# Optimization experiments

Measured on AMD Instinct MI355X. Metric: run time of the kernel, lower is better.

The kernel has to match this reference:

```python
import jax
import jax.numpy as jnp
import numpy as np

L, H_DIM = 8192, 128
ATTN_WINDOW, STRIDE = 3, 2


def setup_inputs() -> dict:
    key = jax.random.key(0)
    k1, k2, k3, k4, k5 = jax.random.split(key, 5)
    input_sequence = jax.random.normal(k1, (L, H_DIM), dtype=jnp.float32)
    # zoh-discretized diagonal decays exp(Lambda*Delta) lie in (0,1)
    Lambda_bar = jax.random.uniform(k2, (H_DIM, H_DIM), dtype=jnp.float32,
                                    minval=0.5, maxval=0.999)
    C_tilde = jax.random.normal(k3, (H_DIM, H_DIM), dtype=jnp.float32) / jnp.sqrt(
        jnp.float32(H_DIM))
    w_q = jax.random.normal(k4, (ATTN_WINDOW, ATTN_WINDOW), dtype=jnp.float32) * 0.1
    D = jax.random.normal(k5, (ATTN_WINDOW,), dtype=jnp.float32)
    return {
        "input_sequence": input_sequence,
        "Lambda_bar": Lambda_bar,
        "C_tilde": C_tilde,
        "w_q": w_q,
        "D": D,
        "attn_window": ATTN_WINDOW,
        "stride": STRIDE,
    }


def reference(input_sequence, Lambda_bar, C_tilde, w_q, D, attn_window, stride):
    # input_sequence: (L, H); Lambda_bar, C_tilde: (H, H); w_q: (W, W); D: (W,)
    Lseq, H = input_sequence.shape
    num_windows = (Lseq - attn_window) // stride + 1
    idx = jnp.arange(num_windows)[:, None] * stride + jnp.arange(attn_window)
    windows = input_sequence[idx]  # (T, W, H)

    # local self-attention per window: x.T @ w_q @ x  -> (T, H, H), axes (t, a, d)
    lsa = jnp.einsum("twa,wv,tvd->tad", windows, w_q, windows)

    # diagonal linear SSM scan over windows, vectorized over both H axes:
    # carry[a, d] = Lambda_bar[a, d] * carry[a, d] + lsa[t, a, d]
    def step(carry, inp):
        carry = Lambda_bar * carry + inp
        return carry, carry

    init = jnp.zeros((H, H), dtype=input_sequence.dtype)
    _, zs = jax.lax.scan(step, init, lsa)  # (T, a, d)

    # original stacks per-d scans on axis=1 giving (T, d, a), then C_tilde @ u
    # contracts d: out[t, h, a] = sum_d C_tilde[h, d] * zs[t, a, d]
    zs_out = jnp.einsum("hd,tad->tha", C_tilde, zs)  # (T, H, H)

    # os = vmap(u.T @ D): (T, H)
    os = jnp.einsum("twh,w->th", windows, D)
    return zs_out, os
```

## Files before the change

kernel.cpp:

```cpp
#include <hip/hip_runtime.h>

#define L_   8192
#define H_   128
#define T_   4095
#define CH_  16
#define NC_  256

typedef __bf16 bf16x8 __attribute__((ext_vector_type(8)));
typedef unsigned short ushort8 __attribute__((ext_vector_type(8)));
typedef float f32x4 __attribute__((ext_vector_type(4)));

__device__ __forceinline__ unsigned short f2bf(float f) {
    unsigned int u = __builtin_bit_cast(unsigned int, f);
    u += 0x7fffu + ((u >> 16) & 1u);
    return (unsigned short)(u >> 16);
}

__global__ __launch_bounds__(256) void pass1_kernel(const float* __restrict__ X,
                                                    const float* __restrict__ Lam,
                                                    const float* __restrict__ wq,
                                                    float* __restrict__ ebuf) {
    __shared__ float y_s[3][128];
    __shared__ float xa_s[3][32];

    const int tid = threadIdx.x;
    const int c   = blockIdx.x;
    const int a0  = blockIdx.y * 32;
    const int a_l = tid & 31;
    const int dg  = tid >> 5;

    float z[16], lam[16];
    {
        const float* lp = Lam + (size_t)(a0 + a_l) * H_ + dg * 16;
        #pragma unroll
        for (int j = 0; j < 16; ++j) { lam[j] = lp[j]; z[j] = 0.f; }
    }
    const float w00 = wq[0], w01 = wq[1], w02 = wq[2];
    const float w10 = wq[3], w11 = wq[4], w12 = wq[5];
    const float w20 = wq[6], w21 = wq[7], w22 = wq[8];

    const int t0 = c * CH_;
    const int t1 = min(t0 + CH_, T_);

    for (int t = t0; t < t1; ++t) {
        __syncthreads();
        const float* xr = X + (size_t)(2 * t) * H_;
        if (tid < 128) {
            float xd0 = xr[tid], xd1 = xr[H_ + tid], xd2 = xr[2 * H_ + tid];
            y_s[0][tid] = w00 * xd0 + w01 * xd1 + w02 * xd2;
            y_s[1][tid] = w10 * xd0 + w11 * xd1 + w12 * xd2;
            y_s[2][tid] = w20 * xd0 + w21 * xd1 + w22 * xd2;
        } else if (tid < 224) {
            int li = tid - 128;
            xa_s[li >> 5][li & 31] = xr[(li >> 5) * H_ + a0 + (li & 31)];
        }
        __syncthreads();
        const float xa0 = xa_s[0][a_l], xa1 = xa_s[1][a_l], xa2 = xa_s[2][a_l];
        #pragma unroll
        for (int j = 0; j < 16; ++j) {
            const int d = dg * 16 + j;
            float u = xa0 * y_s[0][d] + xa1 * y_s[1][d] + xa2 * y_s[2][d];
            z[j] = fmaf(lam[j], z[j], u);
        }
    }
    float* ep = ebuf + (size_t)c * (H_ * H_) + (size_t)(a0 + a_l) * H_ + dg * 16;
    #pragma unroll
    for (int j = 0; j < 16; ++j) ep[j] = z[j];
}

__global__ __launch_bounds__(256) void pass2_kernel(const float* __restrict__ Lam,
                                                    float* __restrict__ ebuf) {
    const int entry = blockIdx.x * 256 + threadIdx.x;
    const float lam = Lam[entry];
    float p = lam * lam; p = p * p; p = p * p; p = p * p;
    float z = 0.f;
    for (int cb = 0; cb < NC_; cb += 8) {
        float tmp[8];
        #pragma unroll
        for (int i = 0; i < 8; ++i)
            tmp[i] = ebuf[(size_t)(cb + i) * (H_ * H_) + entry];
        #pragma unroll
        for (int i = 0; i < 8; ++i) {
            ebuf[(size_t)(cb + i) * (H_ * H_) + entry] = z;
            z = fmaf(p, z, tmp[i]);
        }
    }
}

__global__ __launch_bounds__(256) void pass3_kernel(const float* __restrict__ X,
                                                    const float* __restrict__ Lam,
                                                    const float* __restrict__ Cm,
                                                    const float* __restrict__ wq,
                                                    const float* __restrict__ Dv,
                                                    const float* __restrict__ carry,
                                                    float* __restrict__ out,
                                                    float* __restrict__ os) {
    __shared__ unsigned short z_s[32][136];
    __shared__ float y_s[3][128];
    __shared__ float xa_s[3][32];

    const int tid  = threadIdx.x;
    const int c    = blockIdx.x;
    const int a0   = blockIdx.y * 32;
    const int lane = tid & 63;
    const int wave = tid >> 6;
    const int m    = lane & 15;
    const int q    = lane >> 4;

    ushort8 cfrag[2][4];
    #pragma unroll
    for (int ni = 0; ni < 2; ++ni) {
        const int h = (wave * 2 + ni) * 16 + m;
        #pragma unroll
        for (int kt = 0; kt < 4; ++kt) {
            const float* src = Cm + h * H_ + kt * 32 + q * 8;
            ushort8 v;
            #pragma unroll
            for (int j = 0; j < 8; ++j) v[j] = f2bf(src[j]);
            cfrag[ni][kt] = v;
        }
    }

    const int a_l = tid & 31;
    const int dg  = tid >> 5;
    float z[16], lam[16];
    {
        const float* lp = Lam   + (size_t)(a0 + a_l) * H_ + dg * 16;
        const float* cp = carry + (size_t)c * (H_ * H_) + (size_t)(a0 + a_l) * H_ + dg * 16;
        #pragma unroll
        for (int j = 0; j < 16; ++j) { lam[j] = lp[j]; z[j] = cp[j]; }
    }
    const float w00 = wq[0], w01 = wq[1], w02 = wq[2];
    const float w10 = wq[3], w11 = wq[4], w12 = wq[5];
    const float w20 = wq[6], w21 = wq[7], w22 = wq[8];
    const float d0 = Dv[0], d1 = Dv[1], d2 = Dv[2];
    const bool do_os = (blockIdx.y == 0);

    const int t0 = c * CH_;
    const int t1 = min(t0 + CH_, T_);

    for (int t = t0; t < t1; ++t) {
        __syncthreads();
        const float* xr = X + (size_t)(2 * t) * H_;
        if (tid < 128) {
            float xd0 = xr[tid], xd1 = xr[H_ + tid], xd2 = xr[2 * H_ + tid];
            y_s[0][tid] = w00 * xd0 + w01 * xd1 + w02 * xd2;
            y_s[1][tid] = w10 * xd0 + w11 * xd1 + w12 * xd2;
            y_s[2][tid] = w20 * xd0 + w21 * xd1 + w22 * xd2;
            if (do_os) os[t * H_ + tid] = d0 * xd0 + d1 * xd1 + d2 * xd2;
        } else if (tid < 224) {
            int li = tid - 128;
            xa_s[li >> 5][li & 31] = xr[(li >> 5) * H_ + a0 + (li & 31)];
        }
        __syncthreads();

        {
            const float xa0 = xa_s[0][a_l], xa1 = xa_s[1][a_l], xa2 = xa_s[2][a_l];
            #pragma unroll
            for (int j = 0; j < 16; ++j) {
                const int d = dg * 16 + j;
                float u = xa0 * y_s[0][d] + xa1 * y_s[1][d] + xa2 * y_s[2][d];
                z[j] = fmaf(lam[j], z[j], u);
            }
            ushort8 zb0, zb1;
            #pragma unroll
            for (int j = 0; j < 8; ++j) { zb0[j] = f2bf(z[j]); zb1[j] = f2bf(z[j + 8]); }
            *(ushort8*)&z_s[a_l][dg * 16]     = zb0;
            *(ushort8*)&z_s[a_l][dg * 16 + 8] = zb1;
        }
        __syncthreads();

        f32x4 acc[2][2] = {};
        #pragma unroll
        for (int kt = 0; kt < 4; ++kt) {
            bf16x8 za = __builtin_bit_cast(bf16x8, *(const ushort8*)&z_s[m][kt * 32 + q * 8]);
            bf16x8 zb = __builtin_bit_cast(bf16x8, *(const ushort8*)&z_s[16 + m][kt * 32 + q * 8]);
            #pragma unroll
            for (int ni = 0; ni < 2; ++ni) {
                bf16x8 cf = __builtin_bit_cast(bf16x8, cfrag[ni][kt]);
                acc[0][ni] = __builtin_amdgcn_mfma_f32_16x16x32_bf16(za, cf, acc[0][ni], 0, 0, 0);
                acc[1][ni] = __builtin_amdgcn_mfma_f32_16x16x32_bf16(zb, cf, acc[1][ni], 0, 0, 0);
            }
        }
        float* ob = out + (size_t)t * (H_ * H_) + a0;
        #pragma unroll
        for (int mi = 0; mi < 2; ++mi) {
            #pragma unroll
            for (int ni = 0; ni < 2; ++ni) {
                const int h = (wave * 2 + ni) * 16 + m;
                *(f32x4*)&ob[(size_t)h * H_ + mi * 16 + q * 4] = acc[mi][ni];
            }
        }
    }
}

extern "C" void kernel_launch(void* const* d_in, const int* in_sizes, int n_in,
                              void* d_out, int out_size, void* d_ws, size_t ws_size,
                              hipStream_t stream) {
    const float* X   = (const float*)d_in[0];
    const float* Lam = (const float*)d_in[1];
    const float* Cm  = (const float*)d_in[2];
    const float* wq  = (const float*)d_in[3];
    const float* Dv  = (const float*)d_in[4];
    float* out = (float*)d_out;
    float* os  = out + (size_t)T_ * H_ * H_;
    float* ebuf = (float*)d_ws;

    pass1_kernel<<<dim3(NC_, 4), 256, 0, stream>>>(X, Lam, wq, ebuf);
    pass2_kernel<<<64, 256, 0, stream>>>(Lam, ebuf);
    pass3_kernel<<<dim3(NC_, 4), 256, 0, stream>>>(X, Lam, Cm, wq, Dv, ebuf, out, os);
}
```

Before: 346.6 us.

## Restructure scan passes into sync-free single-wave blocks with precomputed bf16 C fragments

Pass1 and pass3 drop shared memory and barriers. Each thread now loads X rows directly with vector loads and recomputes the w_q projection itself. Pass3 becomes 64-thread blocks over 16-row tiles that keep the bf16 z fragment in registers and feed it straight into MFMA, and a new pass0 pre-packs C into bf16 MFMA fragment layout in workspace. Pass1 skips the last chunk and pass2 turns into an inclusive scan read with a shifted index, which removes unused work. The trade-off is redundant X loads and y computation per thread, plus C fragments reloaded from global memory every timestep.

```diff
diff --git a/kernel.cpp b/kernel.cpp
--- a/kernel.cpp
+++ b/kernel.cpp
@@ -5,6 +5,8 @@
 #define T_   4095
 #define CH_  16
 #define NC_  256
+#define HH_  (H_ * H_)
+#define CBF_OFF ((size_t)(NC_ - 1) * HH_)
 
 typedef __bf16 bf16x8 __attribute__((ext_vector_type(8)));
 typedef unsigned short ushort8 __attribute__((ext_vector_type(8)));
@@ -16,180 +18,184 @@
     return (unsigned short)(u >> 16);
 }
 
+__global__ __launch_bounds__(256) void pass0_kernel(const float* __restrict__ Cm,
+                                                    unsigned short* __restrict__ Cbf) {
+    const int gid  = blockIdx.x * 256 + threadIdx.x;
+    const int frag = gid >> 6, lane = gid & 63;
+    const int nt = frag >> 2, kt = frag & 3;
+    const int n  = nt * 16 + (lane & 15);
+    const int k0 = kt * 32 + (lane >> 4) * 8;
+    const float* src = Cm + (size_t)n * H_ + k0;
+    ushort8 v;
+    #pragma unroll
+    for (int j = 0; j < 8; ++j) v[j] = f2bf(src[j]);
+    *(ushort8*)(Cbf + (size_t)gid * 8) = v;
+}
+
 __global__ __launch_bounds__(256) void pass1_kernel(const float* __restrict__ X,
                                                     const float* __restrict__ Lam,
                                                     const float* __restrict__ wq,
                                                     float* __restrict__ ebuf) {
-    __shared__ float y_s[3][128];
-    __shared__ float xa_s[3][32];
-
     const int tid = threadIdx.x;
     const int c   = blockIdx.x;
-    const int a0  = blockIdx.y * 32;
-    const int a_l = tid & 31;
-    const int dg  = tid >> 5;
-
-    float z[16], lam[16];
+    const int a0  = blockIdx.y * 16;
+    const int a   = a0 + (tid & 15);
+    const int d0  = (tid >> 4) * 8;
+
+    float z[8], lam[8];
     {
-        const float* lp = Lam + (size_t)(a0 + a_l) * H_ + dg * 16;
-        #pragma unroll
-        for (int j = 0; j < 16; ++j) { lam[j] = lp[j]; z[j] = 0.f; }
+        const float* lp = Lam + (size_t)a * H_ + d0;
+        #pragma unroll
+        for (int j = 0; j < 8; ++j) { lam[j] = lp[j]; z[j] = 0.f; }
     }
     const float w00 = wq[0], w01 = wq[1], w02 = wq[2];
     const float w10 = wq[3], w11 = wq[4], w12 = wq[5];
     const float w20 = wq[6], w21 = wq[7], w22 = wq[8];
 
     const int t0 = c * CH_;
-    const int t1 = min(t0 + CH_, T_);
-
-    for (int t = t0; t < t1; ++t) {
-        __syncthreads();
+    for (int t = t0; t < t0 + CH_; ++t) {
         const float* xr = X + (size_t)(2 * t) * H_;
-        if (tid < 128) {
-            float xd0 = xr[tid], xd1 = xr[H_ + tid], xd2 = xr[2 * H_ + tid];
-            y_s[0][tid] = w00 * xd0 + w01 * xd1 + w02 * xd2;
-            y_s[1][tid] = w10 * xd0 + w11 * xd1 + w12 * xd2;
-            y_s[2][tid] = w20 * xd0 + w21 * xd1 + w22 * xd2;
-        } else if (tid < 224) {
-            int li = tid - 128;
-            xa_s[li >> 5][li & 31] = xr[(li >> 5) * H_ + a0 + (li & 31)];
-        }
-        __syncthreads();
-        const float xa0 = xa_s[0][a_l], xa1 = xa_s[1][a_l], xa2 = xa_s[2][a_l];
-        #pragma unroll
-        for (int j = 0; j < 16; ++j) {
-            const int d = dg * 16 + j;
-            float u = xa0 * y_s[0][d] + xa1 * y_s[1][d] + xa2 * y_s[2][d];
-            z[j] = fmaf(lam[j], z[j], u);
-        }
-    }
-    float* ep = ebuf + (size_t)c * (H_ * H_) + (size_t)(a0 + a_l) * H_ + dg * 16;
-    #pragma unroll
-    for (int j = 0; j < 16; ++j) ep[j] = z[j];
+        f32x4 x0a = *(const f32x4*)(xr + d0),           x0b = *(const f32x4*)(xr + d0 + 4);
+        f32x4 x1a = *(const f32x4*)(xr + H_ + d0),      x1b = *(const f32x4*)(xr + H_ + d0 + 4);
+        f32x4 x2a = *(const f32x4*)(xr + 2 * H_ + d0),  x2b = *(const f32x4*)(xr + 2 * H_ + d0 + 4);
+        const float xa0 = xr[a], xa1 = xr[H_ + a], xa2 = xr[2 * H_ + a];
+        #pragma unroll
+        for (int j = 0; j < 4; ++j) {
+            {
+                const float y0 = w00 * x0a[j] + w01 * x1a[j] + w02 * x2a[j];
+                const float y1 = w10 * x0a[j] + w11 * x1a[j] + w12 * x2a[j];
+                const float y2 = w20 * x0a[j] + w21 * x1a[j] + w22 * x2a[j];
+                z[j] = fmaf(lam[j], z[j], xa0 * y0 + xa1 * y1 + xa2 * y2);
+            }
+            {
+                const float y0 = w00 * x0b[j] + w01 * x1b[j] + w02 * x2b[j];
+                const float y1 = w10 * x0b[j] + w11 * x1b[j] + w12 * x2b[j];
+                const float y2 = w20 * x0b[j] + w21 * x1b[j] + w22 * x2b[j];
+                z[j + 4] = fmaf(lam[j + 4], z[j + 4], xa0 * y0 + xa1 * y1 + xa2 * y2);
+            }
+        }
+    }
+    float* ep = ebuf + (size_t)c * HH_ + (size_t)a * H_ + d0;
+    f32x4 zlo = {z[0], z[1], z[2], z[3]};
+    f32x4 zhi = {z[4], z[5], z[6], z[7]};
+    *(f32x4*)ep       = zlo;
+    *(f32x4*)(ep + 4) = zhi;
 }
 
 __global__ __launch_bounds__(256) void pass2_kernel(const float* __restrict__ Lam,
                                                     float* __restrict__ ebuf) {
-    const int entry = blockIdx.x * 256 + threadIdx.x;
-    const float lam = Lam[entry];
-    float p = lam * lam; p = p * p; p = p * p; p = p * p;
+    const int e = blockIdx.x * 256 + threadIdx.x;
+    const float lam = Lam[e];
+    float p2 = lam * lam, p4 = p2 * p2, p8 = p4 * p4;
+    const float l16 = p8 * p8;
     float z = 0.f;
-    for (int cb = 0; cb < NC_; cb += 8) {
+    for (int cb = 0; cb < 248; cb += 8) {
         float tmp[8];
         #pragma unroll
-        for (int i = 0; i < 8; ++i)
-            tmp[i] = ebuf[(size_t)(cb + i) * (H_ * H_) + entry];
+        for (int i = 0; i < 8; ++i) tmp[i] = ebuf[(size_t)(cb + i) * HH_ + e];
         #pragma unroll
         for (int i = 0; i < 8; ++i) {
-            ebuf[(size_t)(cb + i) * (H_ * H_) + entry] = z;
-            z = fmaf(p, z, tmp[i]);
-        }
-    }
-}
-
-__global__ __launch_bounds__(256) void pass3_kernel(const float* __restrict__ X,
-                                                    const float* __restrict__ Lam,
-                                                    const float* __restrict__ Cm,
-                                                    const float* __restrict__ wq,
-                                                    const float* __restrict__ Dv,
-                                                    const float* __restrict__ carry,
-                                                    float* __restrict__ out,
-                                                    float* __restrict__ os) {
-    __shared__ unsigned short z_s[32][136];
-    __shared__ float y_s[3][128];
-    __shared__ float xa_s[3][32];
-
-    const int tid  = threadIdx.x;
+            z = fmaf(l16, z, tmp[i]);
+            ebuf[(size_t)(cb + i) * HH_ + e] = z;
+        }
+    }
+    {
+        float tmp[7];
+        #pragma unroll
+        for (int i = 0; i < 7; ++i) tmp[i] = ebuf[(size_t)(248 + i) * HH_ + e];
+        #pragma unroll
+        for (int i = 0; i < 7; ++i) {
+            z = fmaf(l16, z, tmp[i]);
+            ebuf[(size_t)(248 + i) * HH_ + e] = z;
+        }
+    }
+}
+
+__global__ __launch_bounds__(64, 2) void pass3_kernel(const float* __restrict__ X,
+                                                      const float* __restrict__ Lam,
+                                                      const float* __restrict__ wq,
+                                                      const float* __restrict__ Dv,
+                                                      const float* __restrict__ ws,
+                                                      float* __restrict__ out,
+                                                      float* __restrict__ os) {
+    const int lane = threadIdx.x;
     const int c    = blockIdx.x;
-    const int a0   = blockIdx.y * 32;
-    const int lane = tid & 63;
-    const int wave = tid >> 6;
-    const int m    = lane & 15;
-    const int q    = lane >> 4;
-
-    ushort8 cfrag[2][4];
+    const int a0   = blockIdx.y * 16;
+    const int m    = lane & 15, q = lane >> 4;
+    const int a    = a0 + m;
+    const unsigned short* Cbf = (const unsigned short*)(ws + CBF_OFF);
+
+    float z[4][8], lam[4][8];
     #pragma unroll
-    for (int ni = 0; ni < 2; ++ni) {
-        const int h = (wave * 2 + ni) * 16 + m;
-        #pragma unroll
-        for (int kt = 0; kt < 4; ++kt) {
-            const float* src = Cm + h * H_ + kt * 32 + q * 8;
-            ushort8 v;
-            #pragma unroll
-            for (int j = 0; j < 8; ++j) v[j] = f2bf(src[j]);
-            cfrag[ni][kt] = v;
-        }
-    }
-
-    const int a_l = tid & 31;
-    const int dg  = tid >> 5;
-    float z[16], lam[16];
-    {
-        const float* lp = Lam   + (size_t)(a0 + a_l) * H_ + dg * 16;
-        const float* cp = carry + (size_t)c * (H_ * H_) + (size_t)(a0 + a_l) * H_ + dg * 16;
-        #pragma unroll
-        for (int j = 0; j < 16; ++j) { lam[j] = lp[j]; z[j] = cp[j]; }
+    for (int cc = 0; cc < 4; ++cc) {
+        const int k0 = cc * 32 + q * 8;
+        const float* lp = Lam + (size_t)a * H_ + k0;
+        #pragma unroll
+        for (int j = 0; j < 8; ++j) lam[cc][j] = lp[j];
+        if (c == 0) {
+            #pragma unroll
+            for (int j = 0; j < 8; ++j) z[cc][j] = 0.f;
+        } else {
+            const float* cp = ws + (size_t)(c - 1) * HH_ + (size_t)a * H_ + k0;
+            #pragma unroll
+            for (int j = 0; j < 8; ++j) z[cc][j] = cp[j];
+        }
     }
     const float w00 = wq[0], w01 = wq[1], w02 = wq[2];
     const float w10 = wq[3], w11 = wq[4], w12 = wq[5];
     const float w20 = wq[6], w21 = wq[7], w22 = wq[8];
-    const float d0 = Dv[0], d1 = Dv[1], d2 = Dv[2];
+    const float dv0 = Dv[0], dv1 = Dv[1], dv2 = Dv[2];
     const bool do_os = (blockIdx.y == 0);
 
-    const int t0 = c * CH_;
-    const int t1 = min(t0 + CH_, T_);
-
+    const int t0 = c * CH_, t1 = min(t0 + CH_, T_);
     for (int t = t0; t < t1; ++t) {
-        __syncthreads();
         const float* xr = X + (size_t)(2 * t) * H_;
-        if (tid < 128) {
-            float xd0 = xr[tid], xd1 = xr[H_ + tid], xd2 = xr[2 * H_ + tid];
-            y_s[0][tid] = w00 * xd0 + w01 * xd1 + w02 * xd2;
-            y_s[1][tid] = w10 * xd0 + w11 * xd1 + w12 * xd2;
-            y_s[2][tid] = w20 * xd0 + w21 * xd1 + w22 * xd2;
-            if (do_os) os[t * H_ + tid] = d0 * xd0 + d1 * xd1 + d2 * xd2;
-        } else if (tid < 224) {
-            int li = tid - 128;
-            xa_s[li >> 5][li & 31] = xr[(li >> 5) * H_ + a0 + (li & 31)];
-        }
-        __syncthreads();
-
-        {
-            const float xa0 = xa_s[0][a_l], xa1 = xa_s[1][a_l], xa2 = xa_s[2][a_l];
-            #pragma unroll
-            for (int j = 0; j < 16; ++j) {
-                const int d = dg * 16 + j;
-                float u = xa0 * y_s[0][d] + xa1 * y_s[1][d] + xa2 * y_s[2][d];
-                z[j] = fmaf(lam[j], z[j], u);
-            }
-            ushort8 zb0, zb1;
-            #pragma unroll
-            for (int j = 0; j < 8; ++j) { zb0[j] = f2bf(z[j]); zb1[j] = f2bf(z[j + 8]); }
-            *(ushort8*)&z_s[a_l][dg * 16]     = zb0;
-            *(ushort8*)&z_s[a_l][dg * 16 + 8] = zb1;
-        }
-        __syncthreads();
-
-        f32x4 acc[2][2] = {};
-        #pragma unroll
-        for (int kt = 0; kt < 4; ++kt) {
-            bf16x8 za = __builtin_bit_cast(bf16x8, *(const ushort8*)&z_s[m][kt * 32 + q * 8]);
-            bf16x8 zb = __builtin_bit_cast(bf16x8, *(const ushort8*)&z_s[16 + m][kt * 32 + q * 8]);
-            #pragma unroll
-            for (int ni = 0; ni < 2; ++ni) {
-                bf16x8 cf = __builtin_bit_cast(bf16x8, cfrag[ni][kt]);
-                acc[0][ni] = __builtin_amdgcn_mfma_f32_16x16x32_bf16(za, cf, acc[0][ni], 0, 0, 0);
-                acc[1][ni] = __builtin_amdgcn_mfma_f32_16x16x32_bf16(zb, cf, acc[1][ni], 0, 0, 0);
-            }
-        }
-        float* ob = out + (size_t)t * (H_ * H_) + a0;
-        #pragma unroll
-        for (int mi = 0; mi < 2; ++mi) {
-            #pragma unroll
-            for (int ni = 0; ni < 2; ++ni) {
-                const int h = (wave * 2 + ni) * 16 + m;
-                *(f32x4*)&ob[(size_t)h * H_ + mi * 16 + q * 4] = acc[mi][ni];
-            }
+        const float xa0 = xr[a], xa1 = xr[H_ + a], xa2 = xr[2 * H_ + a];
+        ushort8 za[4];
+        #pragma unroll
+        for (int cc = 0; cc < 4; ++cc) {
+            const int k0 = cc * 32 + q * 8;
+            f32x4 x0a = *(const f32x4*)(xr + k0),          x0b = *(const f32x4*)(xr + k0 + 4);
+            f32x4 x1a = *(const f32x4*)(xr + H_ + k0),     x1b = *(const f32x4*)(xr + H_ + k0 + 4);
+            f32x4 x2a = *(const f32x4*)(xr + 2 * H_ + k0), x2b = *(const f32x4*)(xr + 2 * H_ + k0 + 4);
+            ushort8 zb;
+            #pragma unroll
+            for (int j = 0; j < 4; ++j) {
+                {
+                    const float y0 = w00 * x0a[j] + w01 * x1a[j] + w02 * x2a[j];
+                    const float y1 = w10 * x0a[j] + w11 * x1a[j] + w12 * x2a[j];
+                    const float y2 = w20 * x0a[j] + w21 * x1a[j] + w22 * x2a[j];
+                    z[cc][j] = fmaf(lam[cc][j], z[cc][j], xa0 * y0 + xa1 * y1 + xa2 * y2);
+                    zb[j] = f2bf(z[cc][j]);
+                }
+                {
+                    const float y0 = w00 * x0b[j] + w01 * x1b[j] + w02 * x2b[j];
+                    const float y1 = w10 * x0b[j] + w11 * x1b[j] + w12 * x2b[j];
+                    const float y2 = w20 * x0b[j] + w21 * x1b[j] + w22 * x2b[j];
+                    z[cc][j + 4] = fmaf(lam[cc][j + 4], z[cc][j + 4], xa0 * y0 + xa1 * y1 + xa2 * y2);
+                    zb[j + 4] = f2bf(z[cc][j + 4]);
+                }
+            }
+            za[cc] = zb;
+        }
+        if (do_os) {
+            const float s0 = xr[lane], s1 = xr[H_ + lane], s2 = xr[2 * H_ + lane];
+            os[(size_t)t * H_ + lane] = dv0 * s0 + dv1 * s1 + dv2 * s2;
+            const float u0 = xr[64 + lane], u1 = xr[H_ + 64 + lane], u2 = xr[2 * H_ + 64 + lane];
+            os[(size_t)t * H_ + 64 + lane] = dv0 * u0 + dv1 * u1 + dv2 * u2;
+        }
+        float* ob = out + (size_t)t * HH_ + a0 + q * 4;
+        #pragma unroll
+        for (int nt = 0; nt < 8; ++nt) {
+            f32x4 acc = {0.f, 0.f, 0.f, 0.f};
+            #pragma unroll
+            for (int cc = 0; cc < 4; ++cc) {
+                ushort8 cb = *(const ushort8*)(Cbf + ((size_t)(nt * 4 + cc) * 64 + lane) * 8);
+                acc = __builtin_amdgcn_mfma_f32_16x16x32_bf16(
+                    __builtin_bit_cast(bf16x8, za[cc]),
+                    __builtin_bit_cast(bf16x8, cb), acc, 0, 0, 0);
+            }
+            *(f32x4*)(ob + (size_t)(nt * 16 + m) * H_) = acc;
         }
     }
 }
@@ -202,11 +208,12 @@
     const float* Cm  = (const float*)d_in[2];
     const float* wq  = (const float*)d_in[3];
     const float* Dv  = (const float*)d_in[4];
-    float* out = (float*)d_out;
-    float* os  = out + (size_t)T_ * H_ * H_;
+    float* out  = (float*)d_out;
+    float* os   = out + (size_t)T_ * HH_;
     float* ebuf = (float*)d_ws;
 
-    pass1_kernel<<<dim3(NC_, 4), 256, 0, stream>>>(X, Lam, wq, ebuf);
+    pass0_kernel<<<8, 256, 0, stream>>>(Cm, (unsigned short*)(ebuf + CBF_OFF));
+    pass1_kernel<<<dim3(NC_ - 1, 8), 256, 0, stream>>>(X, Lam, wq, ebuf);
     pass2_kernel<<<64, 256, 0, stream>>>(Lam, ebuf);
-    pass3_kernel<<<dim3(NC_, 4), 256, 0, stream>>>(X, Lam, Cm, wq, Dv, ebuf, out, os);
-}
+    pass3_kernel<<<dim3(NC_, 8), 64, 0, stream>>>(X, Lam, wq, Dv, ebuf, out, os);
+}
```

Measured after the change: 460.0 us. 32.7% more time.
